# Kernel optimization log

Hardware: AMD Instinct MI355X
Metric: run time of the kernel (lower is better)

The kernel has to match this reference:

```python
import jax, jax.numpy as jnp
import numpy as np

B, S, D, H = 2, 2048, 512, 8
HD = D // H
SPARSITY = 0.15
KTOP = max(1, int(S * SPARSITY))          # 307 important rows
HALF_WIN = min(32, S // 4) // 2           # 16 -> window |i-j| <= 16
RC = min(16, S // 8)                      # 16 random links per query token


def setup_inputs() -> dict:
    key = jax.random.key(0)
    ks = jax.random.split(key, 8)
    s = 0.02
    return {
        "x":  jax.random.normal(ks[0], (B, S, D), jnp.float32),
        "Wq": jax.random.normal(ks[1], (D, D), jnp.float32) * s,
        "bq": jnp.zeros((D,), jnp.float32),
        "Wk": jax.random.normal(ks[2], (D, D), jnp.float32) * s,
        "bk": jnp.zeros((D,), jnp.float32),
        "Wv": jax.random.normal(ks[3], (D, D), jnp.float32) * s,
        "bv": jnp.zeros((D,), jnp.float32),
        "Wo": jax.random.normal(ks[4], (D, D), jnp.float32) * s,
        "bo": jnp.zeros((D,), jnp.float32),
        "Ws1": jax.random.normal(ks[5], (D, D // 2), jnp.float32) * s,
        "bs1": jnp.zeros((D // 2,), jnp.float32),
        "Ws2": jax.random.normal(ks[6], (D // 2, 1), jnp.float32) * s,
        "bs2": jnp.zeros((1,), jnp.float32),
        # models torch.randperm(S)[:RC] per (b, i); duplicates are harmless for set-to-1
        "rand_idx": jax.random.randint(ks[7], (B, S, RC), 0, S, jnp.int32),
    }


def _sparse_mask(x, Ws1, bs1, Ws2, bs2, rand_idx):
    # importance scorer: Linear -> ReLU -> Linear -> Sigmoid, squeeze(-1)
    imp = jax.nn.sigmoid(jax.nn.relu(x @ Ws1 + bs1) @ Ws2 + bs2)[..., 0]  # [B,S]
    _, top_idx = jax.lax.top_k(imp, KTOP)                                  # [B,KTOP]
    brange = jnp.arange(B)
    row_imp = jnp.zeros((B, S), bool).at[brange[:, None], top_idx].set(True)
    idx = jnp.arange(S)
    win = jnp.abs(idx[:, None] - idx[None, :]) <= HALF_WIN                 # [S,S]
    rmask = jnp.zeros((B, S, S), bool).at[
        brange[:, None, None], idx[None, :, None], rand_idx].set(True)    # [B,S,S]
    mask = row_imp[:, :, None] | win[None, :, :] | rmask                   # [B,S,S]
    tril = idx[:, None] >= idx[None, :]                                    # causal (mask * (causal==0))
    return mask & tril


def reference(x, Wq, bq, Wk, bk, Wv, bv, Wo, bo, Ws1, bs1, Ws2, bs2, rand_idx):
    allowed = _sparse_mask(x, Ws1, bs1, Ws2, bs2, rand_idx)                # [B,S,S] bool
    q = (x @ Wq + bq).reshape(B, S, H, HD).transpose(0, 2, 1, 3)           # [B,H,S,HD]
    k = (x @ Wk + bk).reshape(B, S, H, HD).transpose(0, 2, 1, 3)
    v = (x @ Wv + bv).reshape(B, S, H, HD).transpose(0, 2, 1, 3)
    scores = jnp.einsum('bhid,bhjd->bhij', q, k) / jnp.sqrt(jnp.float32(HD))
    scores = jnp.where(allowed[:, None, :, :], scores, -jnp.inf)
    attn = jax.nn.softmax(scores, axis=-1)                                 # every row has j=i allowed
    out = jnp.einsum('bhij,bhjd->bhid', attn, v)
    out = out.transpose(0, 2, 1, 3).reshape(B, S, D)
    return out @ Wo + bo
```

## Files before the change

kernel.cpp:

```cpp
#include <hip/hip_runtime.h>
#include <math.h>

typedef unsigned short u16;
typedef unsigned int u32;
typedef unsigned long long u64;
typedef short bf16x8 __attribute__((ext_vector_type(8)));
typedef float f32x4 __attribute__((ext_vector_type(4)));

constexpr int NB = 2, NS = 2048, ND = 512, NH = 8, NHD = 64;
constexpr int NKTOP = 307, NHWIN = 16, NRC = 16;
constexpr int NILIST = 320;
constexpr int NSPAR = NS - NKTOP;
constexpr int NSPAD = 1744;
constexpr int NCHUNK = 8;
constexpr int LDSK64 = 72;
constexpr int PSTR = 72;

__device__ __forceinline__ u16 f2bf(float f) {
  u32 u = __builtin_bit_cast(u32, f);
  u32 r = (u + 0x7FFFu + ((u >> 16) & 1u)) >> 16;
  return (u16)r;
}
__device__ __forceinline__ float bf2f(short v) {
  return __builtin_bit_cast(float, (u32)(u16)v << 16);
}

__global__ __launch_bounds__(256) void csa_prep(const float* __restrict__ W0, const float* __restrict__ W1,
                                                const float* __restrict__ W2, const float* __restrict__ W3,
                                                u16* __restrict__ wt, const float* __restrict__ x,
                                                u16* __restrict__ xb, const float* __restrict__ Ws1,
                                                const float* __restrict__ bs1, const float* __restrict__ Ws2,
                                                float* __restrict__ part) {
  __shared__ float sh[2 * 32 * 68];
  const int tid = threadIdx.x;
  if (blockIdx.x < 256) {
    const int m0 = (blockIdx.x & 63) * 64, n0 = (blockIdx.x >> 6) * 64;
    float(*As)[68] = (float(*)[68])sh;
    float(*Bs)[68] = (float(*)[68])(sh + 32 * 68);
    const int ty = tid >> 4, tx = tid & 15;
    float acc[4][4] = {};
    const int arow = tid & 63, aks = (tid >> 6) * 8;
    const int bk = tid >> 3, bc = (tid & 7) * 8;
    for (int k0 = 0; k0 < ND; k0 += 32) {
      __syncthreads();
      {
        float4 a0 = *(const float4*)(&x[(size_t)(m0 + arow) * ND + k0 + aks]);
        float4 a1 = *(const float4*)(&x[(size_t)(m0 + arow) * ND + k0 + aks + 4]);
        As[aks + 0][arow] = a0.x; As[aks + 1][arow] = a0.y;
        As[aks + 2][arow] = a0.z; As[aks + 3][arow] = a0.w;
        As[aks + 4][arow] = a1.x; As[aks + 5][arow] = a1.y;
        As[aks + 6][arow] = a1.z; As[aks + 7][arow] = a1.w;
      }
      *(float4*)(&Bs[bk][bc]) = *(const float4*)(&Ws1[(size_t)(k0 + bk) * 256 + n0 + bc]);
      *(float4*)(&Bs[bk][bc + 4]) = *(const float4*)(&Ws1[(size_t)(k0 + bk) * 256 + n0 + bc + 4]);
      __syncthreads();
      for (int k = 0; k < 32; k++) {
        float4 av = *(const float4*)(&As[k][ty * 4]);
        float4 bv = *(const float4*)(&Bs[k][tx * 4]);
        float aa[4] = {av.x, av.y, av.z, av.w};
        float bb[4] = {bv.x, bv.y, bv.z, bv.w};
        for (int i = 0; i < 4; i++)
          for (int j = 0; j < 4; j++)
            acc[i][j] += aa[i] * bb[j];
      }
    }
    float4 w2 = *(const float4*)(&Ws2[n0 + tx * 4]);
    float4 b1 = *(const float4*)(&bs1[n0 + tx * 4]);
    for (int i = 0; i < 4; i++) {
      float p = fmaxf(acc[i][0] + b1.x, 0.f) * w2.x + fmaxf(acc[i][1] + b1.y, 0.f) * w2.y +
                fmaxf(acc[i][2] + b1.z, 0.f) * w2.z + fmaxf(acc[i][3] + b1.w, 0.f) * w2.w;
      for (int off = 1; off < 16; off <<= 1) p += __shfl_xor(p, off, 64);
      if (tx == 0) part[(size_t)(m0 + ty * 4 + i) * 4 + (blockIdx.x >> 6)] = p;
    }
  } else if (blockIdx.x < 768) {
    const int cb = blockIdx.x - 256;
    const int w = cb >> 7;
    const int kb = ((cb & 127) >> 4) * 64;
    const int nb = (cb & 15) * 32;
    const float* src = (w == 0) ? W0 : (w == 1) ? W1 : (w == 2) ? W2 : W3;
    float(*tile)[33] = (float(*)[33])sh;
    int tx = tid & 31, ty = tid >> 5;
    for (int i = ty; i < 64; i += 8) tile[i][tx] = src[(size_t)(kb + i) * ND + nb + tx];
    __syncthreads();
    u16* dst = wt + (size_t)w * ND * ND;
    for (int n = ty; n < 32; n += 8) {
      u32 pk = (u32)f2bf(tile[2 * tx][n]) | ((u32)f2bf(tile[2 * tx + 1][n]) << 16);
      *(u32*)(&dst[(size_t)(nb + n) * ND + kb + 2 * tx]) = pk;
    }
  } else {
    const int i = ((blockIdx.x - 768) * 256 + tid) * 8;
    float4 v0 = *(const float4*)(x + i);
    float4 v1 = *(const float4*)(x + i + 4);
    u32 o0 = (u32)f2bf(v0.x) | ((u32)f2bf(v0.y) << 16);
    u32 o1 = (u32)f2bf(v0.z) | ((u32)f2bf(v0.w) << 16);
    u32 o2 = (u32)f2bf(v1.x) | ((u32)f2bf(v1.y) << 16);
    u32 o3 = (u32)f2bf(v1.z) | ((u32)f2bf(v1.w) << 16);
    uint4 o = {o0, o1, o2, o3};
    *(uint4*)(xb + i) = o;
  }
}

__global__ __launch_bounds__(256) void csa_rank(const float* __restrict__ part, int* __restrict__ rowimp) {
  __shared__ float vals[NS];
  const int b = blockIdx.y;
  {
    int t8 = threadIdx.x * 8;
    for (int e = 0; e < 8; e++) {
      float4 pp = *(const float4*)(&part[(size_t)(b * NS + t8 + e) * 4]);
      vals[t8 + e] = (pp.x + pp.y) + (pp.z + pp.w);
    }
  }
  __syncthreads();
  const int wave = threadIdx.x >> 6, lane = threadIdx.x & 63;
  const int s0 = blockIdx.x * 8 + wave * 2;
  const int s1 = s0 + 1;
  const float v0 = vals[s0], v1 = vals[s1];
  int r0 = 0, r1 = 0;
  for (int t = lane; t < NS; t += 64) {
    float u = vals[t];
    r0 += (int)((u > v0) | ((u == v0) & (t < s0)));
    r1 += (int)((u > v1) | ((u == v1) & (t < s1)));
  }
  for (int off = 1; off < 64; off <<= 1) {
    r0 += __shfl_xor(r0, off, 64);
    r1 += __shfl_xor(r1, off, 64);
  }
  if (lane == 0) {
    rowimp[b * NS + s0] = (r0 < NKTOP) ? 1 : 0;
    rowimp[b * NS + s1] = (r1 < NKTOP) ? 1 : 0;
  }
}

__global__ __launch_bounds__(256) void csa_ilist(const int* __restrict__ rowimp, int* __restrict__ ilist,
                                                 int* __restrict__ nlist) {
  __shared__ int cs[256];
  int b = blockIdx.x, t = threadIdx.x;
  int flags[8], sum = 0;
  for (int k = 0; k < 8; k++) {
    flags[k] = rowimp[b * NS + t * 8 + k];
    sum += flags[k];
  }
  cs[t] = sum;
  __syncthreads();
  for (int off = 1; off < 256; off <<= 1) {
    int v = (t >= off) ? cs[t - off] : 0;
    __syncthreads();
    cs[t] += v;
    __syncthreads();
  }
  int pos = cs[t] - sum;
  for (int k = 0; k < 8; k++) {
    int r = t * 8 + k;
    if (flags[k]) ilist[b * NILIST + pos++] = r;
    else nlist[b * NSPAD + (r - pos)] = r;
  }
  if (t < NILIST - NKTOP) ilist[b * NILIST + NKTOP + t] = -1;
  if (t < NSPAD - NSPAR) nlist[b * NSPAD + NSPAR + t] = -1;
}

__global__ __launch_bounds__(256) void csa_gemm_qkv(const u16* __restrict__ xb, const u16* __restrict__ Bt,
                                                    const float* __restrict__ bq, const float* __restrict__ bk,
                                                    const float* __restrict__ bv, u16* __restrict__ qb,
                                                    u16* __restrict__ kb, u16* __restrict__ vtb,
                                                    u16* __restrict__ vb) {
  __shared__ __attribute__((aligned(16))) u16 As[128 * LDSK64];
  __shared__ __attribute__((aligned(16))) u16 Bs[64 * LDSK64];
  const int tid = threadIdx.x;
  const int wave = tid >> 6, lane = tid & 63;
  const int quad = lane >> 4, col = lane & 15;
  const int m0 = blockIdx.x * 128;
  const int n0 = blockIdx.y * 64;
  const f32x4 zf = {0.f, 0.f, 0.f, 0.f};
  f32x4 acc[2][4] = {{zf, zf, zf, zf}, {zf, zf, zf, zf}};
  const int sar = tid >> 1, sak = (tid & 1) * 32;
  const int sbr = tid >> 2, sbk = (tid & 3) * 16;
  for (int k0 = 0; k0 < ND; k0 += 64) {
    __syncthreads();
    {
      const u16* xp = &xb[(size_t)(m0 + sar) * ND + k0 + sak];
      u16* ap = &As[sar * LDSK64 + sak];
      *(uint4*)(ap) = *(const uint4*)(xp);
      *(uint4*)(ap + 8) = *(const uint4*)(xp + 8);
      *(uint4*)(ap + 16) = *(const uint4*)(xp + 16);
      *(uint4*)(ap + 24) = *(const uint4*)(xp + 24);
    }
    *(uint4*)(&Bs[sbr * LDSK64 + sbk]) = *(const uint4*)(&Bt[(size_t)(n0 + sbr) * ND + k0 + sbk]);
    *(uint4*)(&Bs[sbr * LDSK64 + sbk + 8]) = *(const uint4*)(&Bt[(size_t)(n0 + sbr) * ND + k0 + sbk + 8]);
    __syncthreads();
    bf16x8 af[2][2];
    for (int r = 0; r < 2; r++)
      for (int hh = 0; hh < 2; hh++)
        af[r][hh] = *(const bf16x8*)(&As[(wave * 32 + r * 16 + col) * LDSK64 + hh * 32 + quad * 8]);
    for (int c = 0; c < 4; c++) {
      bf16x8 b0 = *(const bf16x8*)(&Bs[(c * 16 + col) * LDSK64 + quad * 8]);
      bf16x8 b1 = *(const bf16x8*)(&Bs[(c * 16 + col) * LDSK64 + 32 + quad * 8]);
      acc[0][c] = __builtin_amdgcn_mfma_f32_16x16x32_bf16(af[0][0], b0, acc[0][c], 0, 0, 0);
      acc[0][c] = __builtin_amdgcn_mfma_f32_16x16x32_bf16(af[0][1], b1, acc[0][c], 0, 0, 0);
      acc[1][c] = __builtin_amdgcn_mfma_f32_16x16x32_bf16(af[1][0], b0, acc[1][c], 0, 0, 0);
      acc[1][c] = __builtin_amdgcn_mfma_f32_16x16x32_bf16(af[1][1], b1, acc[1][c], 0, 0, 0);
    }
  }
  const int w = n0 >> 9;
  const float* bias = (w == 0) ? bq : (w == 1) ? bk : bv;
  for (int c = 0; c < 4; c++) {
    const int ng = n0 + c * 16 + col;
    const int nn = ng & 511, hh = nn >> 6, hd = nn & 63;
    const float bvv = bias[nn];
    for (int r = 0; r < 2; r++) {
      for (int rr = 0; rr < 4; rr++) {
        const int m = m0 + wave * 32 + r * 16 + quad * 4 + rr;
        const int bb = m >> 11, s = m & (NS - 1);
        u16 v16 = f2bf(acc[r][c][rr] + bvv);
        if (w == 0) qb[((size_t)(bb * NH + hh) * NS + s) * NHD + hd] = v16;
        else if (w == 1) kb[((size_t)(bb * NH + hh) * NS + s) * NHD + hd] = v16;
        else {
          vtb[((size_t)(bb * NH + hh) * NHD + hd) * NS + s] = v16;
          vb[((size_t)(bb * NH + hh) * NS + s) * NHD + hd] = v16;
        }
      }
    }
  }
}

__global__ __launch_bounds__(256) void csa_gemm_out(const u16* __restrict__ A, const u16* __restrict__ Bt,
                                                    const float* __restrict__ bias, float* __restrict__ outp) {
  __shared__ __attribute__((aligned(16))) u16 As[64 * LDSK64];
  __shared__ __attribute__((aligned(16))) u16 Bs[64 * LDSK64];
  const int tid = threadIdx.x;
  const int wave = tid >> 6, lane = tid & 63;
  const int quad = lane >> 4, col = lane & 15;
  const int m0 = blockIdx.x * 64;
  const int n0 = blockIdx.y * 64;
  const f32x4 zf = {0.f, 0.f, 0.f, 0.f};
  f32x4 acc[4] = {zf, zf, zf, zf};
  const int sr = tid >> 2, sk = (tid & 3) * 16;
  for (int k0 = 0; k0 < ND; k0 += 64) {
    __syncthreads();
    *(uint4*)(&As[sr * LDSK64 + sk]) = *(const uint4*)(&A[(size_t)(m0 + sr) * ND + k0 + sk]);
    *(uint4*)(&As[sr * LDSK64 + sk + 8]) = *(const uint4*)(&A[(size_t)(m0 + sr) * ND + k0 + sk + 8]);
    *(uint4*)(&Bs[sr * LDSK64 + sk]) = *(const uint4*)(&Bt[(size_t)(n0 + sr) * ND + k0 + sk]);
    *(uint4*)(&Bs[sr * LDSK64 + sk + 8]) = *(const uint4*)(&Bt[(size_t)(n0 + sr) * ND + k0 + sk + 8]);
    __syncthreads();
    bf16x8 af0 = *(const bf16x8*)(&As[(wave * 16 + col) * LDSK64 + quad * 8]);
    bf16x8 af1 = *(const bf16x8*)(&As[(wave * 16 + col) * LDSK64 + 32 + quad * 8]);
    for (int nt = 0; nt < 4; nt++) {
      bf16x8 bf0 = *(const bf16x8*)(&Bs[(nt * 16 + col) * LDSK64 + quad * 8]);
      bf16x8 bf1 = *(const bf16x8*)(&Bs[(nt * 16 + col) * LDSK64 + 32 + quad * 8]);
      acc[nt] = __builtin_amdgcn_mfma_f32_16x16x32_bf16(af0, bf0, acc[nt], 0, 0, 0);
      acc[nt] = __builtin_amdgcn_mfma_f32_16x16x32_bf16(af1, bf1, acc[nt], 0, 0, 0);
    }
  }
  for (int nt = 0; nt < 4; nt++) {
    const int n = n0 + nt * 16 + col;
    const float bvv = bias[n];
    for (int r = 0; r < 4; r++) {
      const int m = m0 + wave * 16 + quad * 4 + r;
      outp[(size_t)m * ND + n] = acc[nt][r] + bvv;
    }
  }
}

__global__ __launch_bounds__(64) void csa_attn_imp(const u16* __restrict__ qb, const u16* __restrict__ kb,
                                                   const u16* __restrict__ vtb, const int* __restrict__ ilist,
                                                   float* __restrict__ pbuf) {
  const int lane = threadIdx.x;
  const int quad = lane >> 4, col = lane & 15;
  const int qt = blockIdx.x;
  const int chunk = blockIdx.y;
  const int bh = blockIdx.z;
  const int b = bh >> 3, h = bh & 7;

  const int* il = ilist + b * NILIST;
  const u16* qptr = qb + (size_t)(b * NH + h) * NS * NHD;
  const u16* kptr = kb + (size_t)(b * NH + h) * NS * NHD;
  const u16* vptr = vtb + (size_t)(b * NH + h) * NHD * NS;

  const int iq = il[qt * 16 + col];
  const int qrow = (iq < 0) ? 0 : iq;
  bf16x8 qf0 = *(const bf16x8*)(qptr + qrow * NHD + quad * 8);
  bf16x8 qf1 = *(const bf16x8*)(qptr + qrow * NHD + 32 + quad * 8);

  const f32x4 zf = {0.f, 0.f, 0.f, 0.f};
  float m_r[4], l_r[4];
  f32x4 of[4];
  int irow[4];
  for (int r = 0; r < 4; r++) {
    m_r[r] = -INFINITY;
    l_r[r] = 0.f;
    irow[r] = il[qt * 16 + quad * 4 + r];
  }
  for (int n = 0; n < 4; n++) of[n] = zf;

  __shared__ __attribute__((aligned(16))) u16 Pl[16 * PSTR];

  const int max_i = il[(qt * 16 + 15 > NKTOP - 1) ? (NKTOP - 1) : (qt * 16 + 15)];
  const int ntiles = (max_i >> 6) + 1;
  for (int t = chunk; t < ntiles; t += NCHUNK) {
    const int j0 = t * 64;
    f32x4 cg[4];
    for (int g = 0; g < 4; g++) {
      const int jb = j0 + g * 16;
      bf16x8 k0f = *(const bf16x8*)(kptr + (jb + col) * NHD + quad * 8);
      bf16x8 k1f = *(const bf16x8*)(kptr + (jb + col) * NHD + 32 + quad * 8);
      f32x4 c = zf;
      c = __builtin_amdgcn_mfma_f32_16x16x32_bf16(qf0, k0f, c, 0, 0, 0);
      c = __builtin_amdgcn_mfma_f32_16x16x32_bf16(qf1, k1f, c, 0, 0, 0);
      cg[g] = c;
    }
    float ps[4][4], alpha[4];
    for (int r = 0; r < 4; r++) {
      const int i = irow[r];
      float s[4];
      float vmax = -INFINITY;
      for (int g = 0; g < 4; g++) {
        s[g] = (j0 + g * 16 + col <= i) ? cg[g][r] * 0.125f : -INFINITY;
        vmax = fmaxf(vmax, s[g]);
      }
      for (int off = 1; off < 16; off <<= 1) vmax = fmaxf(vmax, __shfl_xor(vmax, off, 64));
      float newm = fmaxf(m_r[r], vmax);
      bool dead = (newm == -INFINITY);
      float a = dead ? 1.f : __expf(m_r[r] - newm);
      float psum = 0.f;
      for (int g = 0; g < 4; g++) {
        float p = dead ? 0.f : __expf(s[g] - newm);
        ps[r][g] = p;
        psum += p;
      }
      for (int off = 1; off < 16; off <<= 1) psum += __shfl_xor(psum, off, 64);
      m_r[r] = newm;
      l_r[r] = l_r[r] * a + psum;
      alpha[r] = a;
    }
    for (int n = 0; n < 4; n++)
      for (int r = 0; r < 4; r++) of[n][r] *= alpha[r];
    __syncthreads();
    for (int r = 0; r < 4; r++)
      for (int g = 0; g < 4; g++)
        Pl[(quad * 4 + r) * PSTR + g * 16 + col] = f2bf(ps[r][g]);
    __syncthreads();
    bf16x8 pf0 = *(const bf16x8*)(&Pl[col * PSTR + quad * 8]);
    bf16x8 pf1 = *(const bf16x8*)(&Pl[col * PSTR + 32 + quad * 8]);
    for (int vn = 0; vn < 4; vn++) {
      bf16x8 vf0 = *(const bf16x8*)(vptr + (size_t)(vn * 16 + col) * NS + j0 + quad * 8);
      bf16x8 vf1 = *(const bf16x8*)(vptr + (size_t)(vn * 16 + col) * NS + j0 + 32 + quad * 8);
      of[vn] = __builtin_amdgcn_mfma_f32_16x16x32_bf16(pf0, vf0, of[vn], 0, 0, 0);
      of[vn] = __builtin_amdgcn_mfma_f32_16x16x32_bf16(pf1, vf1, of[vn], 0, 0, 0);
    }
  }
  float* pr = pbuf + ((size_t)(bh * NCHUNK + chunk) * NILIST + qt * 16) * 66;
  for (int r = 0; r < 4; r++) {
    const int row = quad * 4 + r;
    if (col == 0) {
      pr[row * 66 + 0] = m_r[r];
      pr[row * 66 + 1] = l_r[r];
    }
    for (int vn = 0; vn < 4; vn++)
      pr[row * 66 + 2 + vn * 16 + col] = of[vn][r];
  }
}

__global__ __launch_bounds__(64) void csa_merge(const float* __restrict__ pbuf, const int* __restrict__ ilist,
                                                u16* __restrict__ attnb) {
  const int kp = blockIdx.x, h = blockIdx.y, b = blockIdx.z;
  const int lane = threadIdx.x;
  const int z = b * NH + h;
  float mc[NCHUNK], lc[NCHUNK], mstar = -INFINITY;
  for (int c = 0; c < NCHUNK; c++) {
    const float* base = pbuf + ((size_t)(z * NCHUNK + c) * NILIST + kp) * 66;
    mc[c] = base[0];
    lc[c] = base[1];
    mstar = fmaxf(mstar, mc[c]);
  }
  float lsum = 0.f, osum = 0.f;
  for (int c = 0; c < NCHUNK; c++) {
    const float* base = pbuf + ((size_t)(z * NCHUNK + c) * NILIST + kp) * 66;
    float w = (mc[c] == -INFINITY) ? 0.f : __expf(mc[c] - mstar);
    lsum += w * lc[c];
    osum += w * base[2 + lane];
  }
  const int i = ilist[b * NILIST + kp];
  attnb[((size_t)(b * NS + i) * NH + h) * NHD + lane] = f2bf(osum / lsum);
}

__global__ __launch_bounds__(256) void csa_attn_sparse(const u16* __restrict__ qb, const u16* __restrict__ kb,
                                                       const u16* __restrict__ vb, const int* __restrict__ nlist,
                                                       const int* __restrict__ rand_idx, u16* __restrict__ attnb) {
  const int wave = threadIdx.x >> 6, lane = threadIdx.x & 63;
  const int slot = blockIdx.x * 4 + wave;
  const int h = blockIdx.y, b = blockIdx.z;
  const int i = nlist[b * NSPAD + slot];
  const int iv = (i < 0) ? 0 : i;

  const u16* qrow = qb + ((size_t)(b * NH + h) * NS + iv) * NHD;
  const u16* kbase = kb + (size_t)(b * NH + h) * NS * NHD;
  const u16* vbase = vb + (size_t)(b * NH + h) * NS * NHD;

  float sd = bf2f((short)qrow[lane]) * bf2f((short)kbase[(size_t)iv * NHD + lane]);
  for (int off = 1; off < 64; off <<= 1) sd += __shfl_xor(sd, off, 64);
  sd *= 0.125f;

  const int c = lane >> 1, half = lane & 1;
  int j, valid;
  if (c < 16) {
    j = i - NHWIN + c;
    valid = (j >= 0);
  } else {
    const int* rr = rand_idx + ((size_t)b * NS + iv) * NRC;
    const int cr = c - 16;
    j = rr[cr];
    valid = (j <= i - NHWIN - 1);
    for (int cp = 0; cp < cr; cp++) valid &= (rr[cp] != j);
  }
  const int jr = valid ? j : 0;
  float s = 0.f;
  {
    const u16* krow = kbase + (size_t)jr * NHD + half * 32;
    const u16* qh = qrow + half * 32;
    for (int c8 = 0; c8 < 4; c8++) {
      bf16x8 kv = *(const bf16x8*)(krow + c8 * 8);
      bf16x8 qv = *(const bf16x8*)(qh + c8 * 8);
      for (int e = 0; e < 8; e++) s += bf2f(qv[e]) * bf2f(kv[e]);
    }
  }
  s += __shfl_xor(s, 1, 64);
  s = valid ? s * 0.125f : -INFINITY;

  float smax = s;
  for (int off = 1; off < 64; off <<= 1) smax = fmaxf(smax, __shfl_xor(smax, off, 64));
  smax = fmaxf(smax, sd);
  float p = valid ? __expf(s - smax) : 0.f;
  float pd = __expf(sd - smax);
  float pm = (half == 0) ? p : 0.f;
  for (int off = 1; off < 64; off <<= 1) pm += __shfl_xor(pm, off, 64);
  const float lsum = pm + pd;

  float o = pd * bf2f((short)vbase[(size_t)iv * NHD + lane]);
#pragma unroll
  for (int jj = 0; jj < 32; jj++) {
    const float pj = __shfl(p, 2 * jj, 64);
    const int jk = __shfl(jr, 2 * jj, 64);
    o += pj * bf2f((short)vbase[(size_t)jk * NHD + lane]);
  }
  if (i >= 0)
    attnb[((size_t)(b * NS + i) * NH + h) * NHD + lane] = f2bf(o / lsum);
}

extern "C" void kernel_launch(void* const* d_in, const int* in_sizes, int n_in,
                              void* d_out, int out_size, void* d_ws, size_t ws_size,
                              hipStream_t stream) {
  const float* x = (const float*)d_in[0];
  const float* bq = (const float*)d_in[2];
  const float* bk = (const float*)d_in[4];
  const float* bv = (const float*)d_in[6];
  const float* bo = (const float*)d_in[8];
  const float* Ws1 = (const float*)d_in[9];
  const float* bs1 = (const float*)d_in[10];
  const float* Ws2 = (const float*)d_in[11];
  const int* rand_idx = (const int*)d_in[13];
  float* out = (float*)d_out;

  char* p = (char*)d_ws;
  u16* wt = (u16*)p;         p += (size_t)4 * ND * ND * 2;
  u16* xb = (u16*)p;         p += (size_t)NB * NS * ND * 2;
  u16* qbuf = (u16*)p;       p += (size_t)NB * NH * NS * NHD * 2;
  u16* kbuf = (u16*)p;       p += (size_t)NB * NH * NS * NHD * 2;
  u16* vtbuf = (u16*)p;      p += (size_t)NB * NH * NHD * NS * 2;
  u16* vbuf = (u16*)p;       p += (size_t)NB * NH * NS * NHD * 2;
  u16* attnb = (u16*)p;      p += (size_t)NB * NS * ND * 2;
  float* part = (float*)p;   p += (size_t)NB * NS * 4 * 4;
  int* rowimp = (int*)p;     p += (size_t)NB * NS * 4;
  int* ilist = (int*)p;      p += (size_t)NB * NILIST * 4;
  int* nlist = (int*)p;      p += (size_t)NB * NSPAD * 4;
  float* pbuf = (float*)p;

  csa_prep<<<dim3(1792), 256, 0, stream>>>((const float*)d_in[1], (const float*)d_in[3],
                                           (const float*)d_in[5], (const float*)d_in[7], wt,
                                           x, xb, Ws1, bs1, Ws2, part);
  csa_rank<<<dim3(NS / 8, NB), 256, 0, stream>>>(part, rowimp);
  csa_ilist<<<dim3(NB), 256, 0, stream>>>(rowimp, ilist, nlist);

  csa_gemm_qkv<<<dim3(32, 24), 256, 0, stream>>>(xb, wt, bq, bk, bv, qbuf, kbuf, vtbuf, vbuf);

  csa_attn_imp<<<dim3(NILIST / 16, NCHUNK, NB * NH), 64, 0, stream>>>(qbuf, kbuf, vtbuf, ilist, pbuf);
  csa_attn_sparse<<<dim3(NSPAD / 4, NH, NB), 256, 0, stream>>>(qbuf, kbuf, vbuf, nlist, rand_idx, attnb);
  csa_merge<<<dim3(NKTOP, NH, NB), 64, 0, stream>>>(pbuf, ilist, attnb);

  csa_gemm_out<<<dim3(64, 8), 256, 0, stream>>>(attnb, wt + 3 * (size_t)ND * ND, bo, out);
}
```

Before: 216.0 us.

## Remap grids to XCD-aware head swizzle and stage sparse attention operands in LDS

Flattens the launch grids of the QKV GEMM and both attention kernels so that the low bits of the block index select head and batch. Consecutive blocks, which the hardware deals round-robin across the MI355X's chiplets, then cover different heads, and each chiplet's L2 keeps a consistent set of K/V heads. In the sparse attention kernel, the query row is staged in LDS and the probabilities and key indices are stored in LDS rather than broadcast through shuffles. The PV loop reads the index through readfirstlane, which makes the V row address scalar. This adds two block-level barriers in the sparse kernel and relies on assumptions about how blocks are dispatched to chiplets.

```diff
diff --git a/kernel.cpp b/kernel.cpp
--- a/kernel.cpp
+++ b/kernel.cpp
@@ -168,8 +168,11 @@
   const int tid = threadIdx.x;
   const int wave = tid >> 6, lane = tid & 63;
   const int quad = lane >> 4, col = lane & 15;
-  const int m0 = blockIdx.x * 128;
-  const int n0 = blockIdx.y * 64;
+  const int hsw = blockIdx.x & 7;
+  const int rest = blockIdx.x >> 3;
+  const int w = rest >> 5;
+  const int m0 = (rest & 31) * 128;
+  const int n0 = (w * 8 + hsw) * 64;
   const f32x4 zf = {0.f, 0.f, 0.f, 0.f};
   f32x4 acc[2][4] = {{zf, zf, zf, zf}, {zf, zf, zf, zf}};
   const int sar = tid >> 1, sak = (tid & 1) * 32;
@@ -200,7 +203,6 @@
       acc[1][c] = __builtin_amdgcn_mfma_f32_16x16x32_bf16(af[1][1], b1, acc[1][c], 0, 0, 0);
     }
   }
-  const int w = n0 >> 9;
   const float* bias = (w == 0) ? bq : (w == 1) ? bk : bv;
   for (int c = 0; c < 4; c++) {
     const int ng = n0 + c * 16 + col;
@@ -265,10 +267,12 @@
                                                    float* __restrict__ pbuf) {
   const int lane = threadIdx.x;
   const int quad = lane >> 4, col = lane & 15;
-  const int qt = blockIdx.x;
-  const int chunk = blockIdx.y;
-  const int bh = blockIdx.z;
-  const int b = bh >> 3, h = bh & 7;
+  const int h = blockIdx.x & 7;
+  const int b = (blockIdx.x >> 3) & 1;
+  const int rest = blockIdx.x >> 4;
+  const int qt = rest % (NILIST / 16);
+  const int chunk = rest / (NILIST / 16);
+  const int bh = b * NH + h;
 
   const int* il = ilist + b * NILIST;
   const u16* qptr = qb + (size_t)(b * NH + h) * NS * NHD;
@@ -385,9 +389,13 @@
 __global__ __launch_bounds__(256) void csa_attn_sparse(const u16* __restrict__ qb, const u16* __restrict__ kb,
                                                        const u16* __restrict__ vb, const int* __restrict__ nlist,
                                                        const int* __restrict__ rand_idx, u16* __restrict__ attnb) {
+  __shared__ __attribute__((aligned(16))) u16 ql[4][64];
+  __shared__ float pl[4][33];
+  __shared__ int jl[4][33];
   const int wave = threadIdx.x >> 6, lane = threadIdx.x & 63;
-  const int slot = blockIdx.x * 4 + wave;
-  const int h = blockIdx.y, b = blockIdx.z;
+  const int h = blockIdx.x & 7;
+  const int b = (blockIdx.x >> 3) & 1;
+  const int slot = (blockIdx.x >> 4) * 4 + wave;
   const int i = nlist[b * NSPAD + slot];
   const int iv = (i < 0) ? 0 : i;
 
@@ -395,7 +403,10 @@
   const u16* kbase = kb + (size_t)(b * NH + h) * NS * NHD;
   const u16* vbase = vb + (size_t)(b * NH + h) * NS * NHD;
 
-  float sd = bf2f((short)qrow[lane]) * bf2f((short)kbase[(size_t)iv * NHD + lane]);
+  if (lane < 8) *(bf16x8*)(&ql[wave][lane * 8]) = *(const bf16x8*)(qrow + lane * 8);
+  __syncthreads();
+
+  float sd = bf2f((short)ql[wave][lane]) * bf2f((short)kbase[(size_t)iv * NHD + lane]);
   for (int off = 1; off < 64; off <<= 1) sd += __shfl_xor(sd, off, 64);
   sd *= 0.125f;
 
@@ -415,10 +426,9 @@
   float s = 0.f;
   {
     const u16* krow = kbase + (size_t)jr * NHD + half * 32;
-    const u16* qh = qrow + half * 32;
     for (int c8 = 0; c8 < 4; c8++) {
       bf16x8 kv = *(const bf16x8*)(krow + c8 * 8);
-      bf16x8 qv = *(const bf16x8*)(qh + c8 * 8);
+      bf16x8 qv = *(const bf16x8*)(&ql[wave][half * 32 + c8 * 8]);
       for (int e = 0; e < 8; e++) s += bf2f(qv[e]) * bf2f(kv[e]);
     }
   }
@@ -434,11 +444,20 @@
   for (int off = 1; off < 64; off <<= 1) pm += __shfl_xor(pm, off, 64);
   const float lsum = pm + pd;
 
-  float o = pd * bf2f((short)vbase[(size_t)iv * NHD + lane]);
-#pragma unroll
-  for (int jj = 0; jj < 32; jj++) {
-    const float pj = __shfl(p, 2 * jj, 64);
-    const int jk = __shfl(jr, 2 * jj, 64);
+  if (half == 0) {
+    pl[wave][c] = p;
+    jl[wave][c] = jr;
+  }
+  if (lane == 0) {
+    pl[wave][32] = pd;
+    jl[wave][32] = iv;
+  }
+  __syncthreads();
+
+  float o = 0.f;
+  for (int jj = 0; jj < 33; jj++) {
+    const int jk = __builtin_amdgcn_readfirstlane(jl[wave][jj]);
+    const float pj = pl[wave][jj];
     o += pj * bf2f((short)vbase[(size_t)jk * NHD + lane]);
   }
   if (i >= 0)
@@ -479,10 +498,10 @@
   csa_rank<<<dim3(NS / 8, NB), 256, 0, stream>>>(part, rowimp);
   csa_ilist<<<dim3(NB), 256, 0, stream>>>(rowimp, ilist, nlist);
 
-  csa_gemm_qkv<<<dim3(32, 24), 256, 0, stream>>>(xb, wt, bq, bk, bv, qbuf, kbuf, vtbuf, vbuf);
-
-  csa_attn_imp<<<dim3(NILIST / 16, NCHUNK, NB * NH), 64, 0, stream>>>(qbuf, kbuf, vtbuf, ilist, pbuf);
-  csa_attn_sparse<<<dim3(NSPAD / 4, NH, NB), 256, 0, stream>>>(qbuf, kbuf, vbuf, nlist, rand_idx, attnb);
+  csa_gemm_qkv<<<dim3(768), 256, 0, stream>>>(xb, wt, bq, bk, bv, qbuf, kbuf, vtbuf, vbuf);
+
+  csa_attn_imp<<<dim3(2560), 64, 0, stream>>>(qbuf, kbuf, vtbuf, ilist, pbuf);
+  csa_attn_sparse<<<dim3((NSPAD / 4) * NH * NB), 256, 0, stream>>>(qbuf, kbuf, vbuf, nlist, rand_idx, attnb);
   csa_merge<<<dim3(NKTOP, NH, NB), 64, 0, stream>>>(pbuf, ilist, attnb);
 
   csa_gemm_out<<<dim3(64, 8), 256, 0, stream>>>(attnb, wt + 3 * (size_t)ND * ND, bo, out);
```

New measurement: 200.0 us. -7.4%, faster.
